# Performance work log

Hardware: AMD Instinct MI355X
Metric: run time of the kernel (lower is better)

The kernel has to match this reference:

```python
import jax, jax.numpy as jnp
import numpy as np


def shift_2d(x, H, W):
    # x: (B, T=H*W, C); quarter-channel directional shifts (gamma=1/4), C must be divisible by 4
    B, T, C = x.shape
    g = C // 4
    xi = x.reshape(B, H, W, C)
    # group 0: shift right along W (output[..., 1:, :] = input[..., :-1, :])
    s0 = jnp.pad(xi[:, :, : W - 1, 0:g], ((0, 0), (0, 0), (1, 0), (0, 0)))
    # group 1: shift left along W
    s1 = jnp.pad(xi[:, :, 1:, g : 2 * g], ((0, 0), (0, 0), (0, 1), (0, 0)))
    # group 2: shift down along H
    s2 = jnp.pad(xi[:, : H - 1, :, 2 * g : 3 * g], ((0, 0), (1, 0), (0, 0), (0, 0)))
    # group 3: shift up along H
    s3 = jnp.pad(xi[:, 1:, :, 3 * g : 4 * g], ((0, 0), (0, 1), (0, 0), (0, 0)))
    out = jnp.concatenate([s0, s1, s2, s3], axis=-1)  # C == 4*g here
    return out.reshape(B, T, C)


def wkv(w, u, k, v):
    # RWKV v4 WKV recurrence with running-max numerical stabilization.
    # w, u: (C,) ; k, v: (B, T, C) ; returns y: (B, T, C)
    B, T, C = k.shape
    NEG = jnp.float32(-1e38)

    def step(carry, kv):
        p, q, o = carry  # numerator state, denominator state, running log-max
        kt, vt = kv
        no = jnp.maximum(o, u + kt)
        A = jnp.exp(o - no)
        Bc = jnp.exp(u + kt - no)
        y = (A * p + Bc * vt) / (A * q + Bc)
        no2 = jnp.maximum(w + o, kt)
        A2 = jnp.exp(w + o - no2)
        B2 = jnp.exp(kt - no2)
        return (A2 * p + B2 * vt, A2 * q + B2, no2), y

    init = (jnp.zeros((B, C), k.dtype), jnp.zeros((B, C), k.dtype), jnp.full((B, C), NEG, k.dtype))
    kT = jnp.moveaxis(k, 1, 0)
    vT = jnp.moveaxis(v, 1, 0)
    _, yT = jax.lax.scan(step, init, (kT, vT))
    return jnp.moveaxis(yT, 0, 1)


def setup_inputs() -> dict:
    key = jax.random.key(0)
    ks = jax.random.split(key, 7)
    B, H, W, C = 16, 96, 96, 192
    T = H * W
    x = jax.random.normal(ks[0], (B, T, C), jnp.float32)
    Wk = jax.random.normal(ks[1], (C, C), jnp.float32) * 0.02
    Wv = jax.random.normal(ks[2], (C, C), jnp.float32) * 0.02
    Wr = jax.random.normal(ks[3], (C, C), jnp.float32) * 0.02
    Wo = jax.random.normal(ks[4], (C, C), jnp.float32) * 0.02
    spatial_decay = jax.random.normal(ks[5], (3, C), jnp.float32)
    spatial_first = jax.random.normal(ks[6], (3, C), jnp.float32)
    return {"x": x, "Wk": Wk, "Wv": Wv, "Wr": Wr, "Wo": Wo,
            "spatial_decay": spatial_decay, "spatial_first": spatial_first,
            "H": H, "W": W}


def reference(x, Wk, Wv, Wr, Wo, spatial_decay, spatial_first, H, W):
    B, T, C = x.shape
    xs = shift_2d(x, H, W)
    k = xs @ Wk.T
    v = xs @ Wv.T
    sr = jax.nn.sigmoid(xs @ Wr.T)
    w = spatial_decay[0] / T
    u = spatial_first[0] / T
    y = wkv(w, u, k, v)
    return (sr * y) @ Wo.T
```

## Files before the change

kernel.cpp:

```cpp
#include <hip/hip_runtime.h>
#include <hip/hip_bf16.h>

typedef __bf16 bf16x8 __attribute__((ext_vector_type(8)));
typedef float f32x4 __attribute__((ext_vector_type(4)));

using bf = __hip_bfloat16;

constexpr int cB = 16, cH = 96, cW = 96, cC = 192;
constexpr int cT = cH * cW;
constexpr int cM = cB * cT;
constexpr int CH = 96;
constexpr int NS = cT / CH;
constexpr float Tinv = 1.0f / 9216.0f;

__device__ __forceinline__ int swz(int row, int bytecol) {
    return row * 384 + (bytecol ^ ((row & 7) << 4));
}
__device__ __forceinline__ float bflo(unsigned u) { return __uint_as_float(u << 16); }
__device__ __forceinline__ float bfhi(unsigned u) { return __uint_as_float(u & 0xffff0000u); }

__global__ __launch_bounds__(256) void convw_k(
    const float* __restrict__ Wk, const float* __restrict__ Wv,
    const float* __restrict__ Wr, const float* __restrict__ Wo,
    bf* __restrict__ out)
{
    int i = (blockIdx.x * 256 + threadIdx.x) * 8;
    int mat = i / 36864, off = i % 36864;
    const float* s = mat == 0 ? Wk : (mat == 1 ? Wv : (mat == 2 ? Wr : Wo));
    const float4* sp = reinterpret_cast<const float4*>(s + off);
    float4 a0 = sp[0], a1 = sp[1];
    bf16x8 pk;
    pk[0]=(__bf16)a0.x; pk[1]=(__bf16)a0.y; pk[2]=(__bf16)a0.z; pk[3]=(__bf16)a0.w;
    pk[4]=(__bf16)a1.x; pk[5]=(__bf16)a1.y; pk[6]=(__bf16)a1.z; pk[7]=(__bf16)a1.w;
    *reinterpret_cast<bf16x8*>(reinterpret_cast<__bf16*>(out) + i) = pk;
}

template <int MODE>
__global__ __launch_bounds__(512, 2) void gemm_k(
    const void* __restrict__ Ap, const bf* __restrict__ Wb,
    void* __restrict__ O0, void* __restrict__ O1, void* __restrict__ O2)
{
    constexpr int NMAT = (MODE == 0) ? 3 : 1;
    __shared__ char lds[2 * 64 * 384 + 192 * 384];
    const int tid = threadIdx.x, bx = blockIdx.x;
    const int lane = tid & 63, wid = tid >> 6;
    const int wm = wid >> 2, wn = wid & 3;
    const int lr = lane & 15, lq = lane >> 4;

    int rj[3], kbj[3];
#pragma unroll
    for (int j = 0; j < 3; ++j) { int idx = tid + j * 512; rj[j] = idx / 24; kbj[j] = idx % 24; }

    float4 pf[6];
    int4   pi[3];

    for (int mat = 0; mat < NMAT; ++mat) {
        {
            const bf* Wt = Wb + (size_t)mat * 192 * cC;
            char* Bb = &lds[0] + 2 * 64 * 384;
            for (int it = 0; it < 9; ++it) {
                int idx = tid + it * 512;
                int r = idx / 24, kb = idx % 24;
                int4 val = *reinterpret_cast<const int4*>(Wt + r * cC + kb * 8);
                *reinterpret_cast<int4*>(Bb + swz(r, kb * 16)) = val;
            }
        }
        if constexpr (MODE == 0) {
            const float* Af = (const float*)Ap;
#pragma unroll
            for (int j = 0; j < 3; ++j) {
                int gm = bx * 64 + rj[j];
                int b = gm / cT, t = gm % cT, h = t / cW, w = t % cW;
                int grp = kbj[j] / 6;
                int hs = h + (grp == 2 ? -1 : (grp == 3 ? 1 : 0));
                int ws2 = w + (grp == 0 ? -1 : (grp == 1 ? 1 : 0));
                pf[2*j] = float4{0,0,0,0}; pf[2*j+1] = float4{0,0,0,0};
                if (hs >= 0 && hs < cH && ws2 >= 0 && ws2 < cW) {
                    const float4* s = reinterpret_cast<const float4*>(
                        Af + ((size_t)b * cT + (size_t)hs * cW + ws2) * cC + kbj[j] * 8);
                    pf[2*j] = s[0]; pf[2*j+1] = s[1];
                }
            }
#pragma unroll
            for (int j = 0; j < 3; ++j) {
                bf16x8 pk;
                pk[0]=(__bf16)pf[2*j].x; pk[1]=(__bf16)pf[2*j].y; pk[2]=(__bf16)pf[2*j].z; pk[3]=(__bf16)pf[2*j].w;
                pk[4]=(__bf16)pf[2*j+1].x; pk[5]=(__bf16)pf[2*j+1].y; pk[6]=(__bf16)pf[2*j+1].z; pk[7]=(__bf16)pf[2*j+1].w;
                *reinterpret_cast<bf16x8*>(&lds[0] + swz(rj[j], kbj[j] * 16)) = pk;
            }
        } else {
            const bf* Az = (const bf*)Ap;
#pragma unroll
            for (int j = 0; j < 3; ++j)
                pi[j] = *reinterpret_cast<const int4*>(Az + (size_t)(bx * 64 + rj[j]) * cC + kbj[j] * 8);
#pragma unroll
            for (int j = 0; j < 3; ++j)
                *reinterpret_cast<int4*>(&lds[0] + swz(rj[j], kbj[j] * 16)) = pi[j];
        }
        __syncthreads();

        for (int i = 0; i < 9; ++i) {
            const int tix = bx + 256 * i;
            if (i < 8) {
                const int tn = bx + 256 * (i + 1);
                if constexpr (MODE == 0) {
                    const float* Af = (const float*)Ap;
#pragma unroll
                    for (int j = 0; j < 3; ++j) {
                        int gm = tn * 64 + rj[j];
                        int b = gm / cT, t = gm % cT, h = t / cW, w = t % cW;
                        int grp = kbj[j] / 6;
                        int hs = h + (grp == 2 ? -1 : (grp == 3 ? 1 : 0));
                        int ws2 = w + (grp == 0 ? -1 : (grp == 1 ? 1 : 0));
                        pf[2*j] = float4{0,0,0,0}; pf[2*j+1] = float4{0,0,0,0};
                        if (hs >= 0 && hs < cH && ws2 >= 0 && ws2 < cW) {
                            const float4* s = reinterpret_cast<const float4*>(
                                Af + ((size_t)b * cT + (size_t)hs * cW + ws2) * cC + kbj[j] * 8);
                            pf[2*j] = s[0]; pf[2*j+1] = s[1];
                        }
                    }
                } else {
                    const bf* Az = (const bf*)Ap;
#pragma unroll
                    for (int j = 0; j < 3; ++j)
                        pi[j] = *reinterpret_cast<const int4*>(Az + (size_t)(tn * 64 + rj[j]) * cC + kbj[j] * 8);
                }
            }
            char* Ab = &lds[0] + (i & 1) * (64 * 384);
            char* Bb = &lds[0] + 2 * 64 * 384;
            f32x4 acc[2][3] = {};
#pragma unroll
            for (int kk = 0; kk < 6; ++kk) {
                const int bc = kk * 64 + lq * 16;
                bf16x8 af[2], bfr[3];
#pragma unroll
                for (int mt = 0; mt < 2; ++mt)
                    af[mt] = *reinterpret_cast<const bf16x8*>(Ab + swz(wm * 32 + mt * 16 + lr, bc));
#pragma unroll
                for (int nt = 0; nt < 3; ++nt)
                    bfr[nt] = *reinterpret_cast<const bf16x8*>(Bb + swz(wn * 48 + nt * 16 + lr, bc));
#pragma unroll
                for (int mt = 0; mt < 2; ++mt)
#pragma unroll
                    for (int nt = 0; nt < 3; ++nt)
                        acc[mt][nt] = __builtin_amdgcn_mfma_f32_16x16x32_bf16(
                            af[mt], bfr[nt], acc[mt][nt], 0, 0, 0);
            }
            if constexpr (MODE == 0) {
                bf* Os = (bf*)(mat == 0 ? O0 : (mat == 1 ? O1 : O2));
#pragma unroll
                for (int mt = 0; mt < 2; ++mt)
#pragma unroll
                    for (int nt = 0; nt < 3; ++nt)
#pragma unroll
                        for (int j = 0; j < 4; ++j) {
                            int row = tix * 64 + wm * 32 + mt * 16 + lq * 4 + j;
                            int col = wn * 48 + nt * 16 + lr;
                            float v = acc[mt][nt][j];
                            if (mat == 2) v = 1.0f / (1.0f + __expf(-v));
                            Os[(size_t)row * cC + col] = __float2bfloat16(v);
                        }
            } else {
                float* Os = (float*)O0;
#pragma unroll
                for (int mt = 0; mt < 2; ++mt)
#pragma unroll
                    for (int nt = 0; nt < 3; ++nt)
#pragma unroll
                        for (int j = 0; j < 4; ++j) {
                            int row = tix * 64 + wm * 32 + mt * 16 + lq * 4 + j;
                            int col = wn * 48 + nt * 16 + lr;
                            Os[(size_t)row * cC + col] = acc[mt][nt][j];
                        }
            }
            if (i < 8) {
                char* An = &lds[0] + ((i + 1) & 1) * (64 * 384);
                if constexpr (MODE == 0) {
#pragma unroll
                    for (int j = 0; j < 3; ++j) {
                        bf16x8 pk;
                        pk[0]=(__bf16)pf[2*j].x; pk[1]=(__bf16)pf[2*j].y; pk[2]=(__bf16)pf[2*j].z; pk[3]=(__bf16)pf[2*j].w;
                        pk[4]=(__bf16)pf[2*j+1].x; pk[5]=(__bf16)pf[2*j+1].y; pk[6]=(__bf16)pf[2*j+1].z; pk[7]=(__bf16)pf[2*j+1].w;
                        *reinterpret_cast<bf16x8*>(An + swz(rj[j], kbj[j] * 16)) = pk;
                    }
                } else {
#pragma unroll
                    for (int j = 0; j < 3; ++j)
                        *reinterpret_cast<int4*>(An + swz(rj[j], kbj[j] * 16)) = pi[j];
                }
            }
            __syncthreads();
        }
    }
}

__global__ __launch_bounds__(192) void wkv_pass1(
    const bf* __restrict__ k, const bf* __restrict__ v,
    const float* __restrict__ sd,
    float* __restrict__ stP, float* __restrict__ stQ, float* __restrict__ stO)
{
    const int c2 = threadIdx.x % 96, sub = threadIdx.x / 96;
    const int b = blockIdx.y, ch = blockIdx.x * 2 + sub;
    const int c0 = c2 * 2;
    const float w0 = sd[c0] * Tinv, w1 = sd[c0 + 1] * Tinv;
    size_t base = ((size_t)b * cT + (size_t)ch * CH) * cC + c0;
    float p0 = 0.f, q0 = 0.f, o0 = -1e38f;
    float p1 = 0.f, q1 = 0.f, o1 = -1e38f;
    for (int s = 0; s < CH; ++s) {
        unsigned kw = *reinterpret_cast<const unsigned*>(k + base + (size_t)s * cC);
        unsigned vw = *reinterpret_cast<const unsigned*>(v + base + (size_t)s * cC);
        float kt0 = bflo(kw), kt1 = bfhi(kw);
        float vt0 = bflo(vw), vt1 = bfhi(vw);
        float no0 = fmaxf(w0 + o0, kt0);
        float A0 = __expf(w0 + o0 - no0), B0 = __expf(kt0 - no0);
        p0 = A0 * p0 + B0 * vt0; q0 = A0 * q0 + B0; o0 = no0;
        float no1 = fmaxf(w1 + o1, kt1);
        float A1 = __expf(w1 + o1 - no1), B1 = __expf(kt1 - no1);
        p1 = A1 * p1 + B1 * vt1; q1 = A1 * q1 + B1; o1 = no1;
    }
    size_t si = ((size_t)b * NS + ch) * cC + c0;
    *reinterpret_cast<float2*>(stP + si) = make_float2(p0, p1);
    *reinterpret_cast<float2*>(stQ + si) = make_float2(q0, q1);
    *reinterpret_cast<float2*>(stO + si) = make_float2(o0, o1);
}

__global__ __launch_bounds__(192) void wkv_pass2(
    const float* __restrict__ stP, const float* __restrict__ stQ,
    const float* __restrict__ stO, const float* __restrict__ sd,
    float* __restrict__ iP, float* __restrict__ iQ, float* __restrict__ iO)
{
    const int c = threadIdx.x, b = blockIdx.x;
    const float w = sd[c] * Tinv;
    const float Lw = w * (float)CH;
    float p = 0.f, q = 0.f, o = -1e38f;
    size_t si = (size_t)b * NS * cC + c;
    float sp = stP[si], sq = stQ[si], so = stO[si];
    for (int ch = 0; ch < NS; ++ch) {
        float np_ = 0.f, nq_ = 0.f, no_ = -1e38f;
        if (ch + 1 < NS) {
            size_t sj = si + (size_t)(ch + 1) * cC;
            np_ = stP[sj]; nq_ = stQ[sj]; no_ = stO[sj];
        }
        size_t sc = si + (size_t)ch * cC;
        iP[sc] = p; iQ[sc] = q; iO[sc] = o;
        float po = o + Lw;
        float m = fmaxf(po, so);
        float e1 = __expf(po - m), e2 = __expf(so - m);
        p = e1 * p + e2 * sp;
        q = e1 * q + e2 * sq;
        o = m;
        sp = np_; sq = nq_; so = no_;
    }
}

__global__ __launch_bounds__(192) void wkv_pass3(
    const bf* __restrict__ k, const bf* __restrict__ v, const bf* __restrict__ sr,
    const float* __restrict__ sd, const float* __restrict__ sf,
    const float* __restrict__ iP, const float* __restrict__ iQ,
    const float* __restrict__ iO, bf* __restrict__ z)
{
    const int c2 = threadIdx.x % 96, sub = threadIdx.x / 96;
    const int b = blockIdx.y, ch = blockIdx.x * 2 + sub;
    const int c0 = c2 * 2;
    const float w0 = sd[c0] * Tinv, w1 = sd[c0 + 1] * Tinv;
    const float u0 = sf[c0] * Tinv, u1 = sf[c0 + 1] * Tinv;
    size_t si = ((size_t)b * NS + ch) * cC + c0;
    float2 pp = *reinterpret_cast<const float2*>(iP + si);
    float2 qq = *reinterpret_cast<const float2*>(iQ + si);
    float2 oo = *reinterpret_cast<const float2*>(iO + si);
    float p0 = pp.x, q0 = qq.x, o0 = oo.x;
    float p1 = pp.y, q1 = qq.y, o1 = oo.y;
    size_t base = ((size_t)b * cT + (size_t)ch * CH) * cC + c0;
    for (int s = 0; s < CH; ++s) {
        size_t ix = base + (size_t)s * cC;
        unsigned kw = *reinterpret_cast<const unsigned*>(k + ix);
        unsigned vw = *reinterpret_cast<const unsigned*>(v + ix);
        unsigned rw = *reinterpret_cast<const unsigned*>(sr + ix);
        float kt0 = bflo(kw), kt1 = bfhi(kw);
        float vt0 = bflo(vw), vt1 = bfhi(vw);
        float rt0 = bflo(rw), rt1 = bfhi(rw);

        float no0 = fmaxf(o0, u0 + kt0);
        float Ae0 = __expf(o0 - no0), Be0 = __expf(u0 + kt0 - no0);
        float y0 = (Ae0 * p0 + Be0 * vt0) / (Ae0 * q0 + Be0);
        float no1 = fmaxf(o1, u1 + kt1);
        float Ae1 = __expf(o1 - no1), Be1 = __expf(u1 + kt1 - no1);
        float y1 = (Ae1 * p1 + Be1 * vt1) / (Ae1 * q1 + Be1);

        bf z0 = __float2bfloat16(rt0 * y0);
        bf z1 = __float2bfloat16(rt1 * y1);
        unsigned zp = (unsigned)*reinterpret_cast<unsigned short*>(&z0)
                    | ((unsigned)*reinterpret_cast<unsigned short*>(&z1) << 16);
        *reinterpret_cast<unsigned*>(z + ix) = zp;

        float m0 = fmaxf(w0 + o0, kt0);
        float A0 = __expf(w0 + o0 - m0), B0 = __expf(kt0 - m0);
        p0 = A0 * p0 + B0 * vt0; q0 = A0 * q0 + B0; o0 = m0;
        float m1 = fmaxf(w1 + o1, kt1);
        float A1 = __expf(w1 + o1 - m1), B1 = __expf(kt1 - m1);
        p1 = A1 * p1 + B1 * vt1; q1 = A1 * q1 + B1; o1 = m1;
    }
}

extern "C" void kernel_launch(void* const* d_in, const int* in_sizes, int n_in,
                              void* d_out, int out_size, void* d_ws, size_t ws_size,
                              hipStream_t stream)
{
    const float* x  = (const float*)d_in[0];
    const float* Wk = (const float*)d_in[1];
    const float* Wv = (const float*)d_in[2];
    const float* Wr = (const float*)d_in[3];
    const float* Wo = (const float*)d_in[4];
    const float* sd = (const float*)d_in[5];
    const float* sf = (const float*)d_in[6];
    float* out = (float*)d_out;

    const size_t nEl = (size_t)cM * cC;
    bf* kbuf  = (bf*)d_out;
    bf* srbuf = (bf*)d_out + nEl;
    char* ws = (char*)d_ws;
    bf* vbuf = (bf*)ws;
    bf* zbuf = (bf*)(ws + 2 * nEl);
    const size_t stN = (size_t)cB * NS * cC;
    float* stP = (float*)(ws + 4 * nEl);
    float* stQ = stP + stN;
    float* stO = stQ + stN;
    float* iP  = stO + stN;
    float* iQ  = iP + stN;
    float* iO  = iQ + stN;
    bf* wbf = (bf*)(iO + stN);

    convw_k<<<dim3(72), dim3(256), 0, stream>>>(Wk, Wv, Wr, Wo, wbf);
    gemm_k<0><<<dim3(256), dim3(512), 0, stream>>>(x, wbf, kbuf, vbuf, srbuf);
    wkv_pass1<<<dim3(NS / 2, cB), dim3(192), 0, stream>>>(kbuf, vbuf, sd, stP, stQ, stO);
    wkv_pass2<<<dim3(cB), dim3(192), 0, stream>>>(stP, stQ, stO, sd, iP, iQ, iO);
    wkv_pass3<<<dim3(NS / 2, cB), dim3(192), 0, stream>>>(
        kbuf, vbuf, srbuf, sd, sf, iP, iQ, iO, zbuf);
    gemm_k<1><<<dim3(256), dim3(512), 0, stream>>>(
        zbuf, wbf + (size_t)576 * cC, out, nullptr, nullptr);
}
```

Baseline: 245.1 us.

## Split shifted-input GEMM, triple-buffer LDS tiles, shorten WKV chunks, prefetch loads

The first GEMM now computes only K and writes the shifted bf16 input to a workspace buffer. A new mode-2 GEMM reads that buffer to produce V and sigmoid(R), so the fp32 gather and shift are not repeated for every matrix. The GEMM moves from double to triple LDS buffering, with register double-buffered global loads issued two tiles ahead. The WKV chunk length is halved so more blocks run in parallel, pass2 writes its prefix states in place, and passes 1 and 3 prefetch the next timestep's k, v and r. The cost is an extra kernel launch, a write and re-read of the shifted input, and more LDS per block, which can lower occupancy.

```diff
diff --git a/kernel.cpp b/kernel.cpp
--- a/kernel.cpp
+++ b/kernel.cpp
@@ -9,7 +9,7 @@
 constexpr int cB = 16, cH = 96, cW = 96, cC = 192;
 constexpr int cT = cH * cW;
 constexpr int cM = cB * cT;
-constexpr int CH = 96;
+constexpr int CH = 48;
 constexpr int NS = cT / CH;
 constexpr float Tinv = 1.0f / 9216.0f;
 
@@ -40,8 +40,8 @@
     const void* __restrict__ Ap, const bf* __restrict__ Wb,
     void* __restrict__ O0, void* __restrict__ O1, void* __restrict__ O2)
 {
-    constexpr int NMAT = (MODE == 0) ? 3 : 1;
-    __shared__ char lds[2 * 64 * 384 + 192 * 384];
+    constexpr int NMAT = (MODE == 2) ? 2 : 1;
+    __shared__ char lds[3 * 64 * 384 + 192 * 384];
     const int tid = threadIdx.x, bx = blockIdx.x;
     const int lane = tid & 63, wid = tid >> 6;
     const int wm = wid >> 2, wn = wid & 3;
@@ -51,25 +51,15 @@
 #pragma unroll
     for (int j = 0; j < 3; ++j) { int idx = tid + j * 512; rj[j] = idx / 24; kbj[j] = idx % 24; }
 
-    float4 pf[6];
-    int4   pi[3];
-
-    for (int mat = 0; mat < NMAT; ++mat) {
-        {
-            const bf* Wt = Wb + (size_t)mat * 192 * cC;
-            char* Bb = &lds[0] + 2 * 64 * 384;
-            for (int it = 0; it < 9; ++it) {
-                int idx = tid + it * 512;
-                int r = idx / 24, kb = idx % 24;
-                int4 val = *reinterpret_cast<const int4*>(Wt + r * cC + kb * 8);
-                *reinterpret_cast<int4*>(Bb + swz(r, kb * 16)) = val;
-            }
-        }
+    float4 pfA[6], pfB[6];
+    int4   piA[3], piB[3];
+
+    auto loadTile = [&](int tile, float4* pf, int4* pi) {
         if constexpr (MODE == 0) {
             const float* Af = (const float*)Ap;
 #pragma unroll
             for (int j = 0; j < 3; ++j) {
-                int gm = bx * 64 + rj[j];
+                int gm = tile * 64 + rj[j];
                 int b = gm / cT, t = gm % cT, h = t / cW, w = t % cW;
                 int grp = kbj[j] / 6;
                 int hs = h + (grp == 2 ? -1 : (grp == 3 ? 1 : 0));
@@ -81,53 +71,52 @@
                     pf[2*j] = s[0]; pf[2*j+1] = s[1];
                 }
             }
+        } else {
+            const bf* Az = (const bf*)Ap;
+#pragma unroll
+            for (int j = 0; j < 3; ++j)
+                pi[j] = *reinterpret_cast<const int4*>(
+                    Az + (size_t)(tile * 64 + rj[j]) * cC + kbj[j] * 8);
+        }
+    };
+    auto writeTile = [&](int bufIdx, int tile, float4* pf, int4* pi) {
+        char* An = &lds[0] + bufIdx * (64 * 384);
+        if constexpr (MODE == 0) {
+            bf* Xs = (bf*)O1;
 #pragma unroll
             for (int j = 0; j < 3; ++j) {
                 bf16x8 pk;
                 pk[0]=(__bf16)pf[2*j].x; pk[1]=(__bf16)pf[2*j].y; pk[2]=(__bf16)pf[2*j].z; pk[3]=(__bf16)pf[2*j].w;
                 pk[4]=(__bf16)pf[2*j+1].x; pk[5]=(__bf16)pf[2*j+1].y; pk[6]=(__bf16)pf[2*j+1].z; pk[7]=(__bf16)pf[2*j+1].w;
-                *reinterpret_cast<bf16x8*>(&lds[0] + swz(rj[j], kbj[j] * 16)) = pk;
+                *reinterpret_cast<bf16x8*>(An + swz(rj[j], kbj[j] * 16)) = pk;
+                *reinterpret_cast<bf16x8*>(Xs + (size_t)(tile * 64 + rj[j]) * cC + kbj[j] * 8) = pk;
             }
         } else {
-            const bf* Az = (const bf*)Ap;
 #pragma unroll
             for (int j = 0; j < 3; ++j)
-                pi[j] = *reinterpret_cast<const int4*>(Az + (size_t)(bx * 64 + rj[j]) * cC + kbj[j] * 8);
-#pragma unroll
-            for (int j = 0; j < 3; ++j)
-                *reinterpret_cast<int4*>(&lds[0] + swz(rj[j], kbj[j] * 16)) = pi[j];
-        }
+                *reinterpret_cast<int4*>(An + swz(rj[j], kbj[j] * 16)) = pi[j];
+        }
+    };
+
+    for (int mat = 0; mat < NMAT; ++mat) {
+        {
+            const bf* Wt = Wb + (size_t)mat * 192 * cC;
+            char* Bb = &lds[0] + 3 * 64 * 384;
+            for (int it = 0; it < 9; ++it) {
+                int idx = tid + it * 512;
+                int r = idx / 24, kb = idx % 24;
+                int4 val = *reinterpret_cast<const int4*>(Wt + r * cC + kb * 8);
+                *reinterpret_cast<int4*>(Bb + swz(r, kb * 16)) = val;
+            }
+        }
+        loadTile(bx, pfA, piA);
+        writeTile(0, bx, pfA, piA);
+        loadTile(bx + 256, pfB, piB);
         __syncthreads();
 
-        for (int i = 0; i < 9; ++i) {
-            const int tix = bx + 256 * i;
-            if (i < 8) {
-                const int tn = bx + 256 * (i + 1);
-                if constexpr (MODE == 0) {
-                    const float* Af = (const float*)Ap;
-#pragma unroll
-                    for (int j = 0; j < 3; ++j) {
-                        int gm = tn * 64 + rj[j];
-                        int b = gm / cT, t = gm % cT, h = t / cW, w = t % cW;
-                        int grp = kbj[j] / 6;
-                        int hs = h + (grp == 2 ? -1 : (grp == 3 ? 1 : 0));
-                        int ws2 = w + (grp == 0 ? -1 : (grp == 1 ? 1 : 0));
-                        pf[2*j] = float4{0,0,0,0}; pf[2*j+1] = float4{0,0,0,0};
-                        if (hs >= 0 && hs < cH && ws2 >= 0 && ws2 < cW) {
-                            const float4* s = reinterpret_cast<const float4*>(
-                                Af + ((size_t)b * cT + (size_t)hs * cW + ws2) * cC + kbj[j] * 8);
-                            pf[2*j] = s[0]; pf[2*j+1] = s[1];
-                        }
-                    }
-                } else {
-                    const bf* Az = (const bf*)Ap;
-#pragma unroll
-                    for (int j = 0; j < 3; ++j)
-                        pi[j] = *reinterpret_cast<const int4*>(Az + (size_t)(tn * 64 + rj[j]) * cC + kbj[j] * 8);
-                }
-            }
-            char* Ab = &lds[0] + (i & 1) * (64 * 384);
-            char* Bb = &lds[0] + 2 * 64 * 384;
+        auto step = [&](int i, float4* wrF, int4* wrI, float4* ldF, int4* ldI) {
+            char* Ab = &lds[0] + (i % 3) * (64 * 384);
+            char* Bb = &lds[0] + 3 * 64 * 384;
             f32x4 acc[2][3] = {};
 #pragma unroll
             for (int kk = 0; kk < 6; ++kk) {
@@ -146,21 +135,8 @@
                         acc[mt][nt] = __builtin_amdgcn_mfma_f32_16x16x32_bf16(
                             af[mt], bfr[nt], acc[mt][nt], 0, 0, 0);
             }
-            if constexpr (MODE == 0) {
-                bf* Os = (bf*)(mat == 0 ? O0 : (mat == 1 ? O1 : O2));
-#pragma unroll
-                for (int mt = 0; mt < 2; ++mt)
-#pragma unroll
-                    for (int nt = 0; nt < 3; ++nt)
-#pragma unroll
-                        for (int j = 0; j < 4; ++j) {
-                            int row = tix * 64 + wm * 32 + mt * 16 + lq * 4 + j;
-                            int col = wn * 48 + nt * 16 + lr;
-                            float v = acc[mt][nt][j];
-                            if (mat == 2) v = 1.0f / (1.0f + __expf(-v));
-                            Os[(size_t)row * cC + col] = __float2bfloat16(v);
-                        }
-            } else {
+            const int tix = bx + 256 * i;
+            if constexpr (MODE == 1) {
                 float* Os = (float*)O0;
 #pragma unroll
                 for (int mt = 0; mt < 2; ++mt)
@@ -172,25 +148,32 @@
                             int col = wn * 48 + nt * 16 + lr;
                             Os[(size_t)row * cC + col] = acc[mt][nt][j];
                         }
-            }
-            if (i < 8) {
-                char* An = &lds[0] + ((i + 1) & 1) * (64 * 384);
-                if constexpr (MODE == 0) {
-#pragma unroll
-                    for (int j = 0; j < 3; ++j) {
-                        bf16x8 pk;
-                        pk[0]=(__bf16)pf[2*j].x; pk[1]=(__bf16)pf[2*j].y; pk[2]=(__bf16)pf[2*j].z; pk[3]=(__bf16)pf[2*j].w;
-                        pk[4]=(__bf16)pf[2*j+1].x; pk[5]=(__bf16)pf[2*j+1].y; pk[6]=(__bf16)pf[2*j+1].z; pk[7]=(__bf16)pf[2*j+1].w;
-                        *reinterpret_cast<bf16x8*>(An + swz(rj[j], kbj[j] * 16)) = pk;
-                    }
-                } else {
-#pragma unroll
-                    for (int j = 0; j < 3; ++j)
-                        *reinterpret_cast<int4*>(An + swz(rj[j], kbj[j] * 16)) = pi[j];
-                }
-            }
+            } else {
+                const bool sig = (MODE == 2) && (mat == 1);
+                bf* Os = (bf*)((MODE == 0) ? O0 : (mat == 0 ? O0 : O1));
+#pragma unroll
+                for (int mt = 0; mt < 2; ++mt)
+#pragma unroll
+                    for (int nt = 0; nt < 3; ++nt)
+#pragma unroll
+                        for (int j = 0; j < 4; ++j) {
+                            int row = tix * 64 + wm * 32 + mt * 16 + lq * 4 + j;
+                            int col = wn * 48 + nt * 16 + lr;
+                            float v = acc[mt][nt][j];
+                            if (sig) v = 1.0f / (1.0f + __expf(-v));
+                            Os[(size_t)row * cC + col] = __float2bfloat16(v);
+                        }
+            }
+            if (i < 8) writeTile((i + 1) % 3, bx + 256 * (i + 1), wrF, wrI);
+            if (i < 7) loadTile(bx + 256 * (i + 2), ldF, ldI);
             __syncthreads();
-        }
+        };
+
+        for (int ii = 0; ii < 4; ++ii) {
+            step(2 * ii,     pfB, piB, pfA, piA);
+            step(2 * ii + 1, pfA, piA, pfB, piB);
+        }
+        step(8, pfB, piB, pfA, piA);
     }
 }
 
@@ -206,17 +189,23 @@
     size_t base = ((size_t)b * cT + (size_t)ch * CH) * cC + c0;
     float p0 = 0.f, q0 = 0.f, o0 = -1e38f;
     float p1 = 0.f, q1 = 0.f, o1 = -1e38f;
+    unsigned kwc = *reinterpret_cast<const unsigned*>(k + base);
+    unsigned vwc = *reinterpret_cast<const unsigned*>(v + base);
     for (int s = 0; s < CH; ++s) {
-        unsigned kw = *reinterpret_cast<const unsigned*>(k + base + (size_t)s * cC);
-        unsigned vw = *reinterpret_cast<const unsigned*>(v + base + (size_t)s * cC);
-        float kt0 = bflo(kw), kt1 = bfhi(kw);
-        float vt0 = bflo(vw), vt1 = bfhi(vw);
+        unsigned kwn = 0, vwn = 0;
+        if (s + 1 < CH) {
+            kwn = *reinterpret_cast<const unsigned*>(k + base + (size_t)(s + 1) * cC);
+            vwn = *reinterpret_cast<const unsigned*>(v + base + (size_t)(s + 1) * cC);
+        }
+        float kt0 = bflo(kwc), kt1 = bfhi(kwc);
+        float vt0 = bflo(vwc), vt1 = bfhi(vwc);
         float no0 = fmaxf(w0 + o0, kt0);
         float A0 = __expf(w0 + o0 - no0), B0 = __expf(kt0 - no0);
         p0 = A0 * p0 + B0 * vt0; q0 = A0 * q0 + B0; o0 = no0;
         float no1 = fmaxf(w1 + o1, kt1);
         float A1 = __expf(w1 + o1 - no1), B1 = __expf(kt1 - no1);
         p1 = A1 * p1 + B1 * vt1; q1 = A1 * q1 + B1; o1 = no1;
+        kwc = kwn; vwc = vwn;
     }
     size_t si = ((size_t)b * NS + ch) * cC + c0;
     *reinterpret_cast<float2*>(stP + si) = make_float2(p0, p1);
@@ -225,9 +214,8 @@
 }
 
 __global__ __launch_bounds__(192) void wkv_pass2(
-    const float* __restrict__ stP, const float* __restrict__ stQ,
-    const float* __restrict__ stO, const float* __restrict__ sd,
-    float* __restrict__ iP, float* __restrict__ iQ, float* __restrict__ iO)
+    float* __restrict__ stP, float* __restrict__ stQ, float* __restrict__ stO,
+    const float* __restrict__ sd)
 {
     const int c = threadIdx.x, b = blockIdx.x;
     const float w = sd[c] * Tinv;
@@ -242,7 +230,7 @@
             np_ = stP[sj]; nq_ = stQ[sj]; no_ = stO[sj];
         }
         size_t sc = si + (size_t)ch * cC;
-        iP[sc] = p; iQ[sc] = q; iO[sc] = o;
+        stP[sc] = p; stQ[sc] = q; stO[sc] = o;
         float po = o + Lw;
         float m = fmaxf(po, so);
         float e1 = __expf(po - m), e2 = __expf(so - m);
@@ -271,14 +259,20 @@
     float p0 = pp.x, q0 = qq.x, o0 = oo.x;
     float p1 = pp.y, q1 = qq.y, o1 = oo.y;
     size_t base = ((size_t)b * cT + (size_t)ch * CH) * cC + c0;
+    unsigned kwc = *reinterpret_cast<const unsigned*>(k + base);
+    unsigned vwc = *reinterpret_cast<const unsigned*>(v + base);
+    unsigned rwc = *reinterpret_cast<const unsigned*>(sr + base);
     for (int s = 0; s < CH; ++s) {
-        size_t ix = base + (size_t)s * cC;
-        unsigned kw = *reinterpret_cast<const unsigned*>(k + ix);
-        unsigned vw = *reinterpret_cast<const unsigned*>(v + ix);
-        unsigned rw = *reinterpret_cast<const unsigned*>(sr + ix);
-        float kt0 = bflo(kw), kt1 = bfhi(kw);
-        float vt0 = bflo(vw), vt1 = bfhi(vw);
-        float rt0 = bflo(rw), rt1 = bfhi(rw);
+        unsigned kwn = 0, vwn = 0, rwn = 0;
+        if (s + 1 < CH) {
+            size_t nx = base + (size_t)(s + 1) * cC;
+            kwn = *reinterpret_cast<const unsigned*>(k + nx);
+            vwn = *reinterpret_cast<const unsigned*>(v + nx);
+            rwn = *reinterpret_cast<const unsigned*>(sr + nx);
+        }
+        float kt0 = bflo(kwc), kt1 = bfhi(kwc);
+        float vt0 = bflo(vwc), vt1 = bfhi(vwc);
+        float rt0 = bflo(rwc), rt1 = bfhi(rwc);
 
         float no0 = fmaxf(o0, u0 + kt0);
         float Ae0 = __expf(o0 - no0), Be0 = __expf(u0 + kt0 - no0);
@@ -291,7 +285,7 @@
         bf z1 = __float2bfloat16(rt1 * y1);
         unsigned zp = (unsigned)*reinterpret_cast<unsigned short*>(&z0)
                     | ((unsigned)*reinterpret_cast<unsigned short*>(&z1) << 16);
-        *reinterpret_cast<unsigned*>(z + ix) = zp;
+        *reinterpret_cast<unsigned*>(z + base + (size_t)s * cC) = zp;
 
         float m0 = fmaxf(w0 + o0, kt0);
         float A0 = __expf(w0 + o0 - m0), B0 = __expf(kt0 - m0);
@@ -299,6 +293,7 @@
         float m1 = fmaxf(w1 + o1, kt1);
         float A1 = __expf(w1 + o1 - m1), B1 = __expf(kt1 - m1);
         p1 = A1 * p1 + B1 * vt1; q1 = A1 * q1 + B1; o1 = m1;
+        kwc = kwn; vwc = vwn; rwc = rwn;
     }
 }
 
@@ -320,22 +315,22 @@
     bf* srbuf = (bf*)d_out + nEl;
     char* ws = (char*)d_ws;
     bf* vbuf = (bf*)ws;
-    bf* zbuf = (bf*)(ws + 2 * nEl);
+    bf* xsbuf = (bf*)(ws + 2 * nEl);
+    bf* zbuf = xsbuf;
     const size_t stN = (size_t)cB * NS * cC;
     float* stP = (float*)(ws + 4 * nEl);
     float* stQ = stP + stN;
     float* stO = stQ + stN;
-    float* iP  = stO + stN;
-    float* iQ  = iP + stN;
-    float* iO  = iQ + stN;
-    bf* wbf = (bf*)(iO + stN);
+    bf* wbf = (bf*)(stO + stN);
 
     convw_k<<<dim3(72), dim3(256), 0, stream>>>(Wk, Wv, Wr, Wo, wbf);
-    gemm_k<0><<<dim3(256), dim3(512), 0, stream>>>(x, wbf, kbuf, vbuf, srbuf);
+    gemm_k<0><<<dim3(256), dim3(512), 0, stream>>>(x, wbf, kbuf, xsbuf, nullptr);
+    gemm_k<2><<<dim3(256), dim3(512), 0, stream>>>(
+        xsbuf, wbf + (size_t)192 * cC, vbuf, srbuf, nullptr);
     wkv_pass1<<<dim3(NS / 2, cB), dim3(192), 0, stream>>>(kbuf, vbuf, sd, stP, stQ, stO);
-    wkv_pass2<<<dim3(cB), dim3(192), 0, stream>>>(stP, stQ, stO, sd, iP, iQ, iO);
+    wkv_pass2<<<dim3(cB), dim3(192), 0, stream>>>(stP, stQ, stO, sd);
     wkv_pass3<<<dim3(NS / 2, cB), dim3(192), 0, stream>>>(
-        kbuf, vbuf, srbuf, sd, sf, iP, iQ, iO, zbuf);
+        kbuf, vbuf, srbuf, sd, sf, stP, stQ, stO, zbuf);
     gemm_k<1><<<dim3(256), dim3(512), 0, stream>>>(
         zbuf, wbf + (size_t)576 * cC, out, nullptr, nullptr);
 }
```

Result: slower. 274.9 us (+12.2%).
